# Kernel optimization log

Hardware: AMD Instinct MI355X
Metric: run time of the kernel (lower is better)

## Reference

```python
import jax, jax.numpy as jnp
import numpy as np

NUM_EXPERTS = 8
INPUT_SIZE = 2048
OUTPUT_SIZE = 8192
EXPERT_SIZES = np.array([3000, 5000, 4096, 2048, 6000, 4000, 4624, 4000], dtype=np.int64)  # sums to 32768
TOTAL_TOKENS = int(EXPERT_SIZES.sum())


def setup_inputs() -> dict:
    key = jax.random.key(0)
    k_in, k_w = jax.random.split(key)
    inputs = jax.random.normal(k_in, (TOTAL_TOKENS, INPUT_SIZE), dtype=jnp.float32)
    # per-expert Linear weights, torch layout [out, in]
    weights = jax.random.normal(k_w, (NUM_EXPERTS, OUTPUT_SIZE, INPUT_SIZE), dtype=jnp.float32) * 0.02
    expert_size = jnp.asarray(EXPERT_SIZES)
    return {"inputs": inputs, "weights": weights, "expert_size": expert_size}


def reference(inputs, weights, expert_size):
    # Grouped GEMM: split tokens by static per-expert counts, y_i = x_i @ W_i^T, concat.
    sizes = [int(s) for s in np.asarray(expert_size)]
    offsets = np.concatenate([[0], np.cumsum(sizes)])
    outs = []
    for i in range(len(sizes)):
        x_i = inputs[offsets[i]:offsets[i + 1]]  # [n_i, input_size]
        outs.append(jnp.einsum('ti,oi->to', x_i, weights[i]))  # [n_i, output_size]
    return jnp.concatenate(outs, axis=0)  # [total_tokens, output_size]
```

## Files before the change

### kernel.cpp

```cpp
#include <hip/hip_runtime.h>

typedef __bf16 bf16x8 __attribute__((ext_vector_type(8)));
typedef float  f32x4  __attribute__((ext_vector_type(4)));

#define KDIM 2048
#define NDIM 8192
#define MTOT 32768
#define BM 256
#define BN 256
#define BK 64
#define NT 32
#define NMT 131
#define NWG (NMT * 32)

__device__ __forceinline__ void gload_lds16(const void* g, void* l) {
    __builtin_amdgcn_global_load_lds(
        (const __attribute__((address_space(1))) void*)g,
        (__attribute__((address_space(3))) void*)l, 16, 0, 0);
}

__global__ __launch_bounds__(256) void convert_f32_bf16(
    const float* __restrict__ src, __bf16* __restrict__ dst, int n8)
{
    const int stride = gridDim.x * blockDim.x;
    for (int i = blockIdx.x * blockDim.x + threadIdx.x; i < n8; i += stride) {
        const f32x4* p = (const f32x4*)(src + (size_t)i * 8);
        f32x4 a = p[0], b = p[1];
        bf16x8 h;
        #pragma unroll
        for (int j = 0; j < 4; ++j) { h[j] = (__bf16)a[j]; h[4 + j] = (__bf16)b[j]; }
        *(bf16x8*)(dst + (size_t)i * 8) = h;
    }
}

__global__ void __launch_bounds__(512, 2) moe_gemm_8ph(
    const __bf16* __restrict__ A,
    const __bf16* __restrict__ W,
    float* __restrict__ C)
{
    __shared__ __bf16 As[2][BM * BK];
    __shared__ __bf16 Bs[2][BN * BK];

    const int tstart[9] = {0, 12, 32, 48, 56, 80, 96, 115, 131};
    const int offs[9]   = {0, 3000, 8000, 12096, 14144, 20144, 24144, 28768, 32768};

    const int bid = blockIdx.x;
    const int mt = bid >> 5;
    const int nt = bid & 31;

    int e = 0;
    #pragma unroll
    for (int i = 1; i < 8; ++i) e += (mt >= tstart[i]) ? 1 : 0;
    const int row0 = offs[e] + (mt - tstart[e]) * BM;
    int rows = offs[e + 1] - row0;
    if (rows > BM) rows = BM;
    const int col0 = nt * BN;

    const int tid  = threadIdx.x;
    const int lane = tid & 63;
    const int w    = tid >> 6;
    const int wm   = w >> 2;
    const int wn   = w & 3;

    const int lrow = lane >> 3;
    const int csrc = ((lane & 7) ^ lrow) * 8;

    const __bf16 *aX[2], *aY[2], *b0[2], *b1[2];
    int ldsAX[2], ldsAY[2], ldsB0[2], ldsB1[2];
    #pragma unroll
    for (int c = 0; c < 2; ++c) {
        const int q  = w * 2 + c;
        const int tX = q * 8 + (q & 8) * 8;
        const int tY = tX + 64;
        int rX = tX + lrow; rX = (rX < rows) ? rX : 0;
        int rY = tY + lrow; rY = (rY < rows) ? rY : 0;
        aX[c] = A + (size_t)(row0 + rX) * KDIM + csrc;
        aY[c] = A + (size_t)(row0 + rY) * KDIM + csrc;
        b0[c] = W + (size_t)(e * NDIM + col0 + q * 8 + lrow) * KDIM + csrc;
        b1[c] = W + (size_t)(e * NDIM + col0 + 128 + q * 8 + lrow) * KDIM + csrc;
        ldsAX[c] = tX * BK;
        ldsAY[c] = tY * BK;
        ldsB0[c] = (q * 8) * BK;
        ldsB1[c] = (128 + q * 8) * BK;
    }

#define STAGE_AX(p, kt) { gload_lds16(aX[0] + (kt) * BK, &As[p][ldsAX[0]]); \
                          gload_lds16(aX[1] + (kt) * BK, &As[p][ldsAX[1]]); }
#define STAGE_AY(p, kt) { gload_lds16(aY[0] + (kt) * BK, &As[p][ldsAY[0]]); \
                          gload_lds16(aY[1] + (kt) * BK, &As[p][ldsAY[1]]); }
#define STAGE_B0(p, kt) { gload_lds16(b0[0] + (kt) * BK, &Bs[p][ldsB0[0]]); \
                          gload_lds16(b0[1] + (kt) * BK, &Bs[p][ldsB0[1]]); }
#define STAGE_B1(p, kt) { gload_lds16(b1[0] + (kt) * BK, &Bs[p][ldsB1[0]]); \
                          gload_lds16(b1[1] + (kt) * BK, &Bs[p][ldsB1[1]]); }

    const int frow = lane & 15;
    const int g8   = (lane >> 4) * 8;
    const int swc  = (frow & 7) << 3;
    const int ck0  = g8 ^ swc;
    const int ck1  = (32 + g8) ^ swc;
    const int arow = wm * 128 + frow;
    const int brow = wn * 64 + frow;

    f32x4 acc[8][4];
    #pragma unroll
    for (int m = 0; m < 8; ++m)
        #pragma unroll
        for (int n = 0; n < 4; ++n)
            acc[m][n] = (f32x4){0.f, 0.f, 0.f, 0.f};

    bf16x8 bk0[4], bk1[4];

#define RD_B(p) { _Pragma("unroll") for (int n = 0; n < 4; ++n) { \
        bk0[n] = *(const bf16x8*)&Bs[p][(brow + n * 16) * BK + ck0]; \
        bk1[n] = *(const bf16x8*)&Bs[p][(brow + n * 16) * BK + ck1]; } }

#define PHASE(p, j, STAGE) { \
    bf16x8 a00 = *(const bf16x8*)&As[p][(arow + (2 * (j)) * 16) * BK + ck0]; \
    bf16x8 a01 = *(const bf16x8*)&As[p][(arow + (2 * (j)) * 16) * BK + ck1]; \
    bf16x8 a10 = *(const bf16x8*)&As[p][(arow + (2 * (j) + 1) * 16) * BK + ck0]; \
    bf16x8 a11 = *(const bf16x8*)&As[p][(arow + (2 * (j) + 1) * 16) * BK + ck1]; \
    STAGE; \
    __builtin_amdgcn_s_barrier(); \
    asm volatile("s_waitcnt lgkmcnt(0)" ::: "memory"); \
    __builtin_amdgcn_s_setprio(1); \
    _Pragma("unroll") for (int n = 0; n < 4; ++n) { \
        acc[2 * (j)][n]     = __builtin_amdgcn_mfma_f32_16x16x32_bf16(a00, bk0[n], acc[2 * (j)][n], 0, 0, 0); \
        acc[2 * (j) + 1][n] = __builtin_amdgcn_mfma_f32_16x16x32_bf16(a10, bk0[n], acc[2 * (j) + 1][n], 0, 0, 0); \
    } \
    _Pragma("unroll") for (int n = 0; n < 4; ++n) { \
        acc[2 * (j)][n]     = __builtin_amdgcn_mfma_f32_16x16x32_bf16(a01, bk1[n], acc[2 * (j)][n], 0, 0, 0); \
        acc[2 * (j) + 1][n] = __builtin_amdgcn_mfma_f32_16x16x32_bf16(a11, bk1[n], acc[2 * (j) + 1][n], 0, 0, 0); \
    } \
    __builtin_amdgcn_s_setprio(0); }

    STAGE_AX(0, 0); STAGE_AY(0, 0); STAGE_B0(0, 0); STAGE_B1(0, 0);
    STAGE_B0(1, 1); STAGE_B1(1, 1); STAGE_AX(1, 1);
    asm volatile("s_waitcnt vmcnt(6)" ::: "memory");
    __builtin_amdgcn_s_barrier();

    #pragma unroll 1
    for (int i = 0; i < 16; ++i) {
        const int t1 = 2 * i + 1;
        int s2 = 2 * i + 2; if (s2 > NT - 1) s2 = NT - 1;
        int s3 = 2 * i + 3; if (s3 > NT - 1) s3 = NT - 1;

        RD_B(0);
        PHASE(0, 0, STAGE_AY(1, t1));
        PHASE(0, 1, STAGE_B0(0, s2));
        PHASE(0, 2, STAGE_B1(0, s2));
        PHASE(0, 3, { STAGE_AX(0, s2); asm volatile("s_waitcnt vmcnt(6)" ::: "memory"); });

        RD_B(1);
        PHASE(1, 0, STAGE_AY(0, s2));
        PHASE(1, 1, STAGE_B0(1, s3));
        PHASE(1, 2, STAGE_B1(1, s3));
        PHASE(1, 3, { STAGE_AX(1, s3); asm volatile("s_waitcnt vmcnt(6)" ::: "memory"); });
    }

    const int crow = (lane >> 4) * 4;
    const int ccol = lane & 15;
    #pragma unroll
    for (int m = 0; m < 8; ++m) {
        #pragma unroll
        for (int j2 = 0; j2 < 4; ++j2) {
            const int r = wm * 128 + m * 16 + crow + j2;
            if (r < rows) {
                float* dst = C + (size_t)(row0 + r) * NDIM + col0 + wn * 64 + ccol;
                #pragma unroll
                for (int n = 0; n < 4; ++n)
                    dst[n * 16] = acc[m][n][j2];
            }
        }
    }
#undef STAGE_AX
#undef STAGE_AY
#undef STAGE_B0
#undef STAGE_B1
#undef RD_B
#undef PHASE
}

__global__ __launch_bounds__(256) void moe_gemm_f32(
    const float* __restrict__ A, const float* __restrict__ W, float* __restrict__ C)
{
    __shared__ __bf16 Asb[128][64];
    __shared__ __bf16 Bsb[128][64];

    const int tstart[9] = {0, 24, 64, 96, 112, 159, 191, 228, 260};
    const int offs[9]   = {0, 3000, 8000, 12096, 14144, 20144, 24144, 28768, 32768};

    const int mt = blockIdx.y;
    int e = 0;
    #pragma unroll
    for (int i = 1; i < 8; ++i) e += (mt >= tstart[i]) ? 1 : 0;
    const int row0 = offs[e] + (mt - tstart[e]) * 128;
    int rows = offs[e + 1] - row0;
    if (rows > 128) rows = 128;
    const int col0 = blockIdx.x * 128;

    const float* __restrict__ Abase = A + (size_t)row0 * KDIM;
    const float* __restrict__ Wbase = W + ((size_t)e * NDIM + (size_t)col0) * KDIM;

    const int tid  = threadIdx.x;
    const int lane = tid & 63;
    const int wid  = tid >> 6;
    const int wr   = (wid >> 1) * 64;
    const int wc   = (wid & 1) * 64;
    const int srow = tid >> 2;
    const int scol = (tid & 3) * 16;

    f32x4 acc[4][4];
    #pragma unroll
    for (int m = 0; m < 4; ++m)
        #pragma unroll
        for (int n = 0; n < 4; ++n)
            acc[m][n] = (f32x4){0.f, 0.f, 0.f, 0.f};
    const f32x4 fzero = (f32x4){0.f, 0.f, 0.f, 0.f};

    for (int k0 = 0; k0 < KDIM; k0 += 64) {
        __syncthreads();
        #pragma unroll
        for (int rr = 0; rr < 2; ++rr) {
            const int r = srow + rr * 64;
            {
                const bool valid = (r < rows);
                const float* pa = Abase + (size_t)r * KDIM + k0 + scol;
                f32x4 v[4];
                #pragma unroll
                for (int i = 0; i < 4; ++i) v[i] = valid ? *(const f32x4*)(pa + 4 * i) : fzero;
                bf16x8 h0, h1;
                #pragma unroll
                for (int i = 0; i < 8; ++i) {
                    h0[i] = (__bf16)v[i >> 2][i & 3];
                    h1[i] = (__bf16)v[2 + (i >> 2)][i & 3];
                }
                *((bf16x8*)&Asb[r][scol]) = h0;
                *((bf16x8*)&Asb[r][scol + 8]) = h1;
            }
            {
                const float* pb = Wbase + (size_t)r * KDIM + k0 + scol;
                f32x4 v[4];
                #pragma unroll
                for (int i = 0; i < 4; ++i) v[i] = *(const f32x4*)(pb + 4 * i);
                bf16x8 h0, h1;
                #pragma unroll
                for (int i = 0; i < 8; ++i) {
                    h0[i] = (__bf16)v[i >> 2][i & 3];
                    h1[i] = (__bf16)v[2 + (i >> 2)][i & 3];
                }
                *((bf16x8*)&Bsb[r][scol]) = h0;
                *((bf16x8*)&Bsb[r][scol + 8]) = h1;
            }
        }
        __syncthreads();
        #pragma unroll
        for (int ks = 0; ks < 2; ++ks) {
            const int kb = ks * 32 + (lane >> 4) * 8;
            bf16x8 af[4], bfr[4];
            #pragma unroll
            for (int m = 0; m < 4; ++m)
                af[m] = *((const bf16x8*)&Asb[wr + m * 16 + (lane & 15)][kb]);
            #pragma unroll
            for (int n = 0; n < 4; ++n)
                bfr[n] = *((const bf16x8*)&Bsb[wc + n * 16 + (lane & 15)][kb]);
            #pragma unroll
            for (int m = 0; m < 4; ++m)
                #pragma unroll
                for (int n = 0; n < 4; ++n)
                    acc[m][n] = __builtin_amdgcn_mfma_f32_16x16x32_bf16(
                        af[m], bfr[n], acc[m][n], 0, 0, 0);
        }
    }

    const int crow = (lane >> 4) * 4;
    const int ccol = lane & 15;
    #pragma unroll
    for (int m = 0; m < 4; ++m) {
        #pragma unroll
        for (int j = 0; j < 4; ++j) {
            const int r = wr + m * 16 + crow + j;
            if (r < rows) {
                float* dst = C + (size_t)(row0 + r) * NDIM + col0 + wc + ccol;
                #pragma unroll
                for (int n = 0; n < 4; ++n)
                    dst[n * 16] = acc[m][n][j];
            }
        }
    }
}

extern "C" void kernel_launch(void* const* d_in, const int* in_sizes, int n_in,
                              void* d_out, int out_size, void* d_ws, size_t ws_size,
                              hipStream_t stream) {
    const float* A = (const float*)d_in[0];
    const float* W = (const float*)d_in[1];
    float* C = (float*)d_out;

    const size_t nA = (size_t)MTOT * KDIM;
    const size_t nW = (size_t)8 * NDIM * KDIM;
    const size_t WS_NEED = (nA + nW) * 2;

    if (ws_size >= WS_NEED) {
        __bf16* Abf = (__bf16*)d_ws;
        __bf16* Wbf = (__bf16*)((char*)d_ws + nA * 2);
        hipLaunchKernelGGL(convert_f32_bf16, dim3(2048), dim3(256), 0, stream,
                           A, Abf, (int)(nA / 8));
        hipLaunchKernelGGL(convert_f32_bf16, dim3(2048), dim3(256), 0, stream,
                           W, Wbf, (int)(nW / 8));
        hipLaunchKernelGGL(moe_gemm_8ph, dim3(NWG), dim3(512), 0, stream,
                           Abf, Wbf, C);
    } else {
        hipLaunchKernelGGL(moe_gemm_f32, dim3(NDIM / 128, 260), dim3(256), 0, stream,
                           A, W, C);
    }
}
```

Measured before the change: 1.483 ms.

## Make grouped GEMM persistent with cross-tile prefetch of next M-tile

Result: slower. 1.659 ms (+11.9%).

```diff
diff --git a/kernel.cpp b/kernel.cpp
--- a/kernel.cpp
+++ b/kernel.cpp
@@ -11,7 +11,6 @@
 #define BK 64
 #define NT 32
 #define NMT 131
-#define NWG (NMT * 32)
 
 __device__ __forceinline__ void gload_lds16(const void* g, void* l) {
     __builtin_amdgcn_global_load_lds(
@@ -33,7 +32,7 @@
     }
 }
 
-__global__ void __launch_bounds__(512, 2) moe_gemm_8ph(
+__global__ void __launch_bounds__(512, 2) moe_gemm_pers(
     const __bf16* __restrict__ A,
     const __bf16* __restrict__ W,
     float* __restrict__ C)
@@ -44,17 +43,9 @@
     const int tstart[9] = {0, 12, 32, 48, 56, 80, 96, 115, 131};
     const int offs[9]   = {0, 3000, 8000, 12096, 14144, 20144, 24144, 28768, 32768};
 
-    const int bid = blockIdx.x;
-    const int mt = bid >> 5;
-    const int nt = bid & 31;
-
-    int e = 0;
-    #pragma unroll
-    for (int i = 1; i < 8; ++i) e += (mt >= tstart[i]) ? 1 : 0;
-    const int row0 = offs[e] + (mt - tstart[e]) * BM;
-    int rows = offs[e + 1] - row0;
-    if (rows > BM) rows = BM;
-    const int col0 = nt * BN;
+    const int xslot = blockIdx.x & 7;
+    const int ntb   = blockIdx.x >> 3;
+    const int col0  = ntb * BN;
 
     const int tid  = threadIdx.x;
     const int lane = tid & 63;
@@ -65,33 +56,17 @@
     const int lrow = lane >> 3;
     const int csrc = ((lane & 7) ^ lrow) * 8;
 
-    const __bf16 *aX[2], *aY[2], *b0[2], *b1[2];
-    int ldsAX[2], ldsAY[2], ldsB0[2], ldsB1[2];
+    int tX[2], tY[2], ldsAX[2], ldsAY[2], ldsB0[2], ldsB1[2];
     #pragma unroll
     for (int c = 0; c < 2; ++c) {
-        const int q  = w * 2 + c;
-        const int tX = q * 8 + (q & 8) * 8;
-        const int tY = tX + 64;
-        int rX = tX + lrow; rX = (rX < rows) ? rX : 0;
-        int rY = tY + lrow; rY = (rY < rows) ? rY : 0;
-        aX[c] = A + (size_t)(row0 + rX) * KDIM + csrc;
-        aY[c] = A + (size_t)(row0 + rY) * KDIM + csrc;
-        b0[c] = W + (size_t)(e * NDIM + col0 + q * 8 + lrow) * KDIM + csrc;
-        b1[c] = W + (size_t)(e * NDIM + col0 + 128 + q * 8 + lrow) * KDIM + csrc;
-        ldsAX[c] = tX * BK;
-        ldsAY[c] = tY * BK;
+        const int q = w * 2 + c;
+        tX[c] = q * 8 + (q & 8) * 8;
+        tY[c] = tX[c] + 64;
+        ldsAX[c] = tX[c] * BK;
+        ldsAY[c] = tY[c] * BK;
         ldsB0[c] = (q * 8) * BK;
         ldsB1[c] = (128 + q * 8) * BK;
     }
-
-#define STAGE_AX(p, kt) { gload_lds16(aX[0] + (kt) * BK, &As[p][ldsAX[0]]); \
-                          gload_lds16(aX[1] + (kt) * BK, &As[p][ldsAX[1]]); }
-#define STAGE_AY(p, kt) { gload_lds16(aY[0] + (kt) * BK, &As[p][ldsAY[0]]); \
-                          gload_lds16(aY[1] + (kt) * BK, &As[p][ldsAY[1]]); }
-#define STAGE_B0(p, kt) { gload_lds16(b0[0] + (kt) * BK, &Bs[p][ldsB0[0]]); \
-                          gload_lds16(b0[1] + (kt) * BK, &Bs[p][ldsB0[1]]); }
-#define STAGE_B1(p, kt) { gload_lds16(b1[0] + (kt) * BK, &Bs[p][ldsB1[0]]); \
-                          gload_lds16(b1[1] + (kt) * BK, &Bs[p][ldsB1[1]]); }
 
     const int frow = lane & 15;
     const int g8   = (lane >> 4) * 8;
@@ -100,15 +75,24 @@
     const int ck1  = (32 + g8) ^ swc;
     const int arow = wm * 128 + frow;
     const int brow = wn * 64 + frow;
+    const int crow = (lane >> 4) * 4;
+    const int ccol = lane & 15;
 
     f32x4 acc[8][4];
-    #pragma unroll
-    for (int m = 0; m < 8; ++m)
-        #pragma unroll
-        for (int n = 0; n < 4; ++n)
-            acc[m][n] = (f32x4){0.f, 0.f, 0.f, 0.f};
-
     bf16x8 bk0[4], bk1[4];
+
+    const __bf16 *aXc[2], *aYc[2], *b0c[2], *b1c[2];
+    const __bf16 *aXn[2], *aYn[2], *b0n[2], *b1n[2];
+
+#define FILL_SET(aX_, aY_, b0_, b1_, row0v, rowsv, ev) { \
+    _Pragma("unroll") for (int c = 0; c < 2; ++c) { \
+        int rX = tX[c] + lrow; rX = (rX < (rowsv)) ? rX : 0; \
+        int rY = tY[c] + lrow; rY = (rY < (rowsv)) ? rY : 0; \
+        aX_[c] = A + (size_t)((row0v) + rX) * KDIM + csrc; \
+        aY_[c] = A + (size_t)((row0v) + rY) * KDIM + csrc; \
+        b0_[c] = W + (size_t)((ev) * NDIM + col0 + (w * 2 + c) * 8 + lrow) * KDIM + csrc; \
+        b1_[c] = W + (size_t)((ev) * NDIM + col0 + 128 + (w * 2 + c) * 8 + lrow) * KDIM + csrc; \
+    } }
 
 #define RD_B(p) { _Pragma("unroll") for (int n = 0; n < 4; ++n) { \
         bk0[n] = *(const bf16x8*)&Bs[p][(brow + n * 16) * BK + ck0]; \
@@ -133,51 +117,112 @@
     } \
     __builtin_amdgcn_s_setprio(0); }
 
-    STAGE_AX(0, 0); STAGE_AY(0, 0); STAGE_B0(0, 0); STAGE_B1(0, 0);
-    STAGE_B0(1, 1); STAGE_B1(1, 1); STAGE_AX(1, 1);
-    asm volatile("s_waitcnt vmcnt(6)" ::: "memory");
-    __builtin_amdgcn_s_barrier();
+#define PSA(Pc, Pn, c) ((i < 15) ? (Pc)[c] + s2o : (Pn)[c])
+#define PSB(Pc, Pn, c) ((i < 15) ? (Pc)[c] + s3o : (Pn)[c] + BK)
+
+    bool first = true;
 
     #pragma unroll 1
-    for (int i = 0; i < 16; ++i) {
-        const int t1 = 2 * i + 1;
-        int s2 = 2 * i + 2; if (s2 > NT - 1) s2 = NT - 1;
-        int s3 = 2 * i + 3; if (s3 > NT - 1) s3 = NT - 1;
-
-        RD_B(0);
-        PHASE(0, 0, STAGE_AY(1, t1));
-        PHASE(0, 1, STAGE_B0(0, s2));
-        PHASE(0, 2, STAGE_B1(0, s2));
-        PHASE(0, 3, { STAGE_AX(0, s2); asm volatile("s_waitcnt vmcnt(6)" ::: "memory"); });
-
-        RD_B(1);
-        PHASE(1, 0, STAGE_AY(0, s2));
-        PHASE(1, 1, STAGE_B0(1, s3));
-        PHASE(1, 2, STAGE_B1(1, s3));
-        PHASE(1, 3, { STAGE_AX(1, s3); asm volatile("s_waitcnt vmcnt(6)" ::: "memory"); });
-    }
-
-    const int crow = (lane >> 4) * 4;
-    const int ccol = lane & 15;
-    #pragma unroll
-    for (int m = 0; m < 8; ++m) {
-        #pragma unroll
-        for (int j2 = 0; j2 < 4; ++j2) {
-            const int r = wm * 128 + m * 16 + crow + j2;
-            if (r < rows) {
-                float* dst = C + (size_t)(row0 + r) * NDIM + col0 + wn * 64 + ccol;
-                #pragma unroll
-                for (int n = 0; n < 4; ++n)
-                    dst[n * 16] = acc[m][n][j2];
-            }
-        }
-    }
-#undef STAGE_AX
-#undef STAGE_AY
-#undef STAGE_B0
-#undef STAGE_B1
+    for (int t = 0;; ++t) {
+        const int mt = t * 8 + xslot;
+        if (mt >= NMT) break;
+
+        int e = 0;
+        #pragma unroll
+        for (int i = 1; i < 8; ++i) e += (mt >= tstart[i]) ? 1 : 0;
+        const int row0 = offs[e] + (mt - tstart[e]) * BM;
+        int rows = offs[e + 1] - row0;
+        if (rows > BM) rows = BM;
+        FILL_SET(aXc, aYc, b0c, b1c, row0, rows, e);
+
+        int mtn = mt + 8;
+        if (mtn >= NMT) mtn = mt;
+        int en = 0;
+        #pragma unroll
+        for (int i = 1; i < 8; ++i) en += (mtn >= tstart[i]) ? 1 : 0;
+        const int row0n = offs[en] + (mtn - tstart[en]) * BM;
+        int rowsn = offs[en + 1] - row0n;
+        if (rowsn > BM) rowsn = BM;
+        FILL_SET(aXn, aYn, b0n, b1n, row0n, rowsn, en);
+
+        #pragma unroll
+        for (int m = 0; m < 8; ++m)
+            #pragma unroll
+            for (int n = 0; n < 4; ++n)
+                acc[m][n] = (f32x4){0.f, 0.f, 0.f, 0.f};
+
+        if (first) {
+            first = false;
+            #pragma unroll
+            for (int c = 0; c < 2; ++c) {
+                gload_lds16(aXc[c], &As[0][ldsAX[c]]);
+                gload_lds16(aYc[c], &As[0][ldsAY[c]]);
+            }
+            #pragma unroll
+            for (int c = 0; c < 2; ++c) {
+                gload_lds16(b0c[c], &Bs[0][ldsB0[c]]);
+                gload_lds16(b1c[c], &Bs[0][ldsB1[c]]);
+            }
+            #pragma unroll
+            for (int c = 0; c < 2; ++c) {
+                gload_lds16(b0c[c] + BK, &Bs[1][ldsB0[c]]);
+                gload_lds16(b1c[c] + BK, &Bs[1][ldsB1[c]]);
+            }
+            #pragma unroll
+            for (int c = 0; c < 2; ++c)
+                gload_lds16(aXc[c] + BK, &As[1][ldsAX[c]]);
+            asm volatile("s_waitcnt vmcnt(6)" ::: "memory");
+            __builtin_amdgcn_s_barrier();
+        }
+
+        #pragma unroll 1
+        for (int i = 0; i < 16; ++i) {
+            const int t1o = (2 * i + 1) * BK;
+            const int s2o = (2 * i + 2) * BK;
+            const int s3o = (2 * i + 3) * BK;
+
+            RD_B(0);
+            PHASE(0, 0, { gload_lds16(aYc[0] + t1o, &As[1][ldsAY[0]]);
+                          gload_lds16(aYc[1] + t1o, &As[1][ldsAY[1]]); });
+            PHASE(0, 1, { gload_lds16(PSA(b0c, b0n, 0), &Bs[0][ldsB0[0]]);
+                          gload_lds16(PSA(b0c, b0n, 1), &Bs[0][ldsB0[1]]); });
+            PHASE(0, 2, { gload_lds16(PSA(b1c, b1n, 0), &Bs[0][ldsB1[0]]);
+                          gload_lds16(PSA(b1c, b1n, 1), &Bs[0][ldsB1[1]]); });
+            PHASE(0, 3, { gload_lds16(PSA(aXc, aXn, 0), &As[0][ldsAX[0]]);
+                          gload_lds16(PSA(aXc, aXn, 1), &As[0][ldsAX[1]]);
+                          asm volatile("s_waitcnt vmcnt(6)" ::: "memory"); });
+
+            RD_B(1);
+            PHASE(1, 0, { gload_lds16(PSA(aYc, aYn, 0), &As[0][ldsAY[0]]);
+                          gload_lds16(PSA(aYc, aYn, 1), &As[0][ldsAY[1]]); });
+            PHASE(1, 1, { gload_lds16(PSB(b0c, b0n, 0), &Bs[1][ldsB0[0]]);
+                          gload_lds16(PSB(b0c, b0n, 1), &Bs[1][ldsB0[1]]); });
+            PHASE(1, 2, { gload_lds16(PSB(b1c, b1n, 0), &Bs[1][ldsB1[0]]);
+                          gload_lds16(PSB(b1c, b1n, 1), &Bs[1][ldsB1[1]]); });
+            PHASE(1, 3, { gload_lds16(PSB(aXc, aXn, 0), &As[1][ldsAX[0]]);
+                          gload_lds16(PSB(aXc, aXn, 1), &As[1][ldsAX[1]]);
+                          asm volatile("s_waitcnt vmcnt(6)" ::: "memory"); });
+        }
+
+        #pragma unroll
+        for (int m = 0; m < 8; ++m) {
+            #pragma unroll
+            for (int j2 = 0; j2 < 4; ++j2) {
+                const int r = wm * 128 + m * 16 + crow + j2;
+                if (r < rows) {
+                    float* dst = C + (size_t)(row0 + r) * NDIM + col0 + wn * 64 + ccol;
+                    #pragma unroll
+                    for (int n = 0; n < 4; ++n)
+                        dst[n * 16] = acc[m][n][j2];
+                }
+            }
+        }
+    }
+#undef FILL_SET
 #undef RD_B
 #undef PHASE
+#undef PSA
+#undef PSB
 }
 
 __global__ __launch_bounds__(256) void moe_gemm_f32(
@@ -307,7 +352,7 @@
                            A, Abf, (int)(nA / 8));
         hipLaunchKernelGGL(convert_f32_bf16, dim3(2048), dim3(256), 0, stream,
                            W, Wbf, (int)(nW / 8));
-        hipLaunchKernelGGL(moe_gemm_8ph, dim3(NWG), dim3(512), 0, stream,
+        hipLaunchKernelGGL(moe_gemm_pers, dim3(256), dim3(512), 0, stream,
                            Abf, Wbf, C);
     } else {
         hipLaunchKernelGGL(moe_gemm_f32, dim3(NDIM / 128, 260), dim3(256), 0, stream,
```
